# Performance work log

Measured on AMD Instinct MI355X. Metric: run time of the kernel, lower is better.

The kernel has to match this reference:

```python
import jax, jax.numpy as jnp
import numpy as np

# Standard minigrid color mapping (module references global COLOR_TO_IDX)
COLOR_TO_IDX = {'red': 0, 'green': 1, 'blue': 2, 'purple': 3, 'yellow': 4, 'grey': 5}
AGENT_FEATURE_SIZE = 13
NUM_AGENTS_PER_COLOR = {'grey': 4, 'yellow': 4}
COLOR_ORDER = sorted(NUM_AGENTS_PER_COLOR.keys())  # ['grey', 'yellow']
FEATURE_DIM = 256
B, N = 131072, 16
INPUT_DIM = (1 + sum(NUM_AGENTS_PER_COLOR.values())) * AGENT_FEATURE_SIZE  # 117


def setup_inputs() -> dict:
    key = jax.random.key(0)
    ks = jax.random.split(key, 14)
    inp = {
        'query_position': jax.random.normal(ks[0], (B, 2), jnp.float32),
        'query_direction': jax.random.normal(ks[1], (B, 4), jnp.float32),
        'query_abilities': jax.random.normal(ks[2], (B, 2), jnp.float32),
        'query_carried': jax.random.normal(ks[3], (B, 2), jnp.float32),
        'query_status': jax.random.normal(ks[4], (B, 3), jnp.float32),
        'all_agent_positions': jax.random.normal(ks[5], (B, N, 2), jnp.float32),
        'all_agent_directions': jax.random.normal(ks[6], (B, N, 4), jnp.float32),
        'all_agent_abilities': jax.random.normal(ks[7], (B, N, 2), jnp.float32),
        'all_agent_carried': jax.random.normal(ks[8], (B, N, 2), jnp.float32),
        'all_agent_status': jax.random.normal(ks[9], (B, N, 3), jnp.float32),
        'agent_color_indices': jax.random.randint(ks[10], (B, N), 0, 6, jnp.int32),
        # fc params; W stored (in, out) so y = x @ W + b (same math as torch Linear)
        'W': jax.random.normal(ks[11], (INPUT_DIM, FEATURE_DIM), jnp.float32) / np.sqrt(INPUT_DIM),
        'b': jax.random.normal(ks[12], (FEATURE_DIM,), jnp.float32) * 0.01,
    }
    return inp


def reference(query_position, query_direction, query_abilities, query_carried,
              query_status, all_agent_positions, all_agent_directions,
              all_agent_abilities, all_agent_carried, all_agent_status,
              agent_color_indices, W, b):
    batch = query_position.shape[0]
    # (B, N, 13) per-agent features, (B, 13) query features
    F = jnp.concatenate([all_agent_positions, all_agent_directions,
                         all_agent_abilities, all_agent_carried,
                         all_agent_status], axis=-1)
    query = jnp.concatenate([query_position, query_direction, query_abilities,
                             query_carried, query_status], axis=-1)
    feats = [query]
    rows = jnp.arange(batch)[:, None]  # (B, 1) for batched scatter
    for color in COLOR_ORDER:
        cidx = COLOR_TO_IDX[color]
        M = NUM_AGENTS_PER_COLOR[color]
        mask = agent_color_indices == cidx                 # (B, N)
        rank = jnp.cumsum(mask, axis=1) - 1                # slot of each matching agent
        valid = mask & (rank < M)
        slot = jnp.where(valid, rank, M)                   # dump overflow/non-match into slot M
        out = jnp.zeros((batch, M + 1, AGENT_FEATURE_SIZE), F.dtype)
        out = out.at[rows, slot].set(F)                    # unique (b, slot) per valid agent
        feats.append(out[:, :M].reshape(batch, M * AGENT_FEATURE_SIZE))
    x = jnp.concatenate(feats, axis=1)                     # (B, 117)
    return jax.nn.relu(x @ W + b)
```

## Files before the change

kernel.cpp:

```cpp
#include <hip/hip_runtime.h>


#define TM 128
#define XS_LD 136
#define THREADS 512
#define NCOL 256
#define KDIM 117

typedef short short8 __attribute__((ext_vector_type(8)));
typedef float f32x4 __attribute__((ext_vector_type(4)));

__device__ __forceinline__ short f2bf(float x) {
    unsigned u = __builtin_bit_cast(unsigned, x);
    unsigned r = (u + 0x7fffu + ((u >> 16) & 1u)) >> 16;
    return (short)r;
}

__global__ __launch_bounds__(THREADS, 2)
void mga_encoder_kernel(const float* __restrict__ qpos, const float* __restrict__ qdir,
                        const float* __restrict__ qabil, const float* __restrict__ qcarr,
                        const float* __restrict__ qstat,
                        const float* __restrict__ apos, const float* __restrict__ adir,
                        const float* __restrict__ aabil, const float* __restrict__ acarr,
                        const float* __restrict__ astat,
                        const int* __restrict__ cidx,
                        const float* __restrict__ W, const float* __restrict__ bvec,
                        float* __restrict__ out) {
    __shared__ __align__(16) short Xs[TM * XS_LD];

    const int tid  = threadIdx.x;
    const int wave = tid >> 6;
    const int lane = tid & 63;
    const int ln   = lane & 15;
    const int q    = lane >> 4;
    const int row0 = blockIdx.x * TM;

    const int r0w = (wave & 1) * 64;
    const int c0  = (wave >> 1) * 64;

    short8 bfr[4][4];
    #pragma unroll
    for (int kt = 0; kt < 4; kt++) {
        #pragma unroll
        for (int ct = 0; ct < 4; ct++) {
            short8 f;
            #pragma unroll
            for (int j = 0; j < 8; j++) {
                int k = kt * 32 + q * 8 + j;
                float wv = (k < KDIM) ? W[(size_t)k * NCOL + c0 + ct * 16 + ln] : 0.f;
                f[j] = f2bf(wv);
            }
            bfr[kt][ct] = f;
        }
    }
    float bv[4];
    #pragma unroll
    for (int ct = 0; ct < 4; ct++) bv[ct] = bvec[c0 + ct * 16 + ln];

    {
        unsigned* z = (unsigned*)Xs;
        #pragma unroll
        for (int i = 0; i < 17; i++) z[tid + THREADS * i] = 0u;
    }
    __syncthreads();

    {
        const int j  = tid & 15;
        const int rr = tid >> 4;
        const int grp = lane & 0x30;
        const unsigned long long rowmask = 0xFFFFull << grp;
        const unsigned long long below   = (1ull << lane) - 1ull;

        int cs[4];
        #pragma unroll
        for (int p = 0; p < 4; p++)
            cs[p] = cidx[((size_t)(row0 + p * 32 + rr)) * 16 + j];

        #pragma unroll
        for (int p = 0; p < 4; p++) {
            const int r = p * 32 + rr;
            const size_t b = (size_t)(row0 + r);
            const int c = cs[p];
            const bool isg = (c == 5);
            const bool isy = (c == 4);
            const unsigned long long bg = __ballot(isg);
            const unsigned long long by = __ballot(isy);
            if (isg | isy) {
                const unsigned long long bal = isg ? bg : by;
                const int rank = __popcll(bal & rowmask & below);
                if (rank < 4) {
                    const int dst = (isg ? 13 : 65) + rank * 13;
                    short* xrow = &Xs[r * XS_LD];
                    const size_t a = b * 16 + (size_t)j;
                    const float2 pp  = ((const float2*)apos)[a];
                    const float4 dd  = ((const float4*)adir)[a];
                    const float2 ab  = ((const float2*)aabil)[a];
                    const float2 ca  = ((const float2*)acarr)[a];
                    const float s0 = astat[a * 3 + 0];
                    const float s1 = astat[a * 3 + 1];
                    const float s2 = astat[a * 3 + 2];
                    xrow[dst + 0]  = f2bf(pp.x);
                    xrow[dst + 1]  = f2bf(pp.y);
                    xrow[dst + 2]  = f2bf(dd.x);
                    xrow[dst + 3]  = f2bf(dd.y);
                    xrow[dst + 4]  = f2bf(dd.z);
                    xrow[dst + 5]  = f2bf(dd.w);
                    xrow[dst + 6]  = f2bf(ab.x);
                    xrow[dst + 7]  = f2bf(ab.y);
                    xrow[dst + 8]  = f2bf(ca.x);
                    xrow[dst + 9]  = f2bf(ca.y);
                    xrow[dst + 10] = f2bf(s0);
                    xrow[dst + 11] = f2bf(s1);
                    xrow[dst + 12] = f2bf(s2);
                }
            }
        }
    }
    if (tid < TM) {
        const size_t b = (size_t)(row0 + tid);
        short* xrow = &Xs[tid * XS_LD];
        const float2 qp = ((const float2*)qpos)[b];
        const float4 qd = ((const float4*)qdir)[b];
        const float2 qa = ((const float2*)qabil)[b];
        const float2 qc = ((const float2*)qcarr)[b];
        const float s0 = qstat[b * 3 + 0];
        const float s1 = qstat[b * 3 + 1];
        const float s2 = qstat[b * 3 + 2];
        xrow[0]  = f2bf(qp.x);  xrow[1]  = f2bf(qp.y);
        xrow[2]  = f2bf(qd.x);  xrow[3]  = f2bf(qd.y);
        xrow[4]  = f2bf(qd.z);  xrow[5]  = f2bf(qd.w);
        xrow[6]  = f2bf(qa.x);  xrow[7]  = f2bf(qa.y);
        xrow[8]  = f2bf(qc.x);  xrow[9]  = f2bf(qc.y);
        xrow[10] = f2bf(s0);    xrow[11] = f2bf(s1);    xrow[12] = f2bf(s2);
    }
    __syncthreads();

    f32x4 acc[4][4];
    #pragma unroll
    for (int rt = 0; rt < 4; rt++)
        #pragma unroll
        for (int ct = 0; ct < 4; ct++) acc[rt][ct] = (f32x4){0.f, 0.f, 0.f, 0.f};

    #pragma unroll
    for (int kt = 0; kt < 4; kt++) {
        short8 av[4];
        #pragma unroll
        for (int rt = 0; rt < 4; rt++)
            av[rt] = *(const short8*)&Xs[(r0w + rt * 16 + ln) * XS_LD + kt * 32 + q * 8];
        #pragma unroll
        for (int rt = 0; rt < 4; rt++)
            #pragma unroll
            for (int ct = 0; ct < 4; ct++)
                acc[rt][ct] = __builtin_amdgcn_mfma_f32_16x16x32_bf16(
                    av[rt], bfr[kt][ct], acc[rt][ct], 0, 0, 0);
    }

    #pragma unroll
    for (int rt = 0; rt < 4; rt++) {
        #pragma unroll
        for (int ct = 0; ct < 4; ct++) {
            #pragma unroll
            for (int i = 0; i < 4; i++) {
                int row = row0 + r0w + rt * 16 + q * 4 + i;
                int col = c0 + ct * 16 + ln;
                float v = acc[rt][ct][i] + bv[ct];
                out[(size_t)row * NCOL + col] = fmaxf(v, 0.f);
            }
        }
    }
}

extern "C" void kernel_launch(void* const* d_in, const int* in_sizes, int n_in,
                              void* d_out, int out_size, void* d_ws, size_t ws_size,
                              hipStream_t stream) {
    const float* qpos  = (const float*)d_in[0];
    const float* qdir  = (const float*)d_in[1];
    const float* qabil = (const float*)d_in[2];
    const float* qcarr = (const float*)d_in[3];
    const float* qstat = (const float*)d_in[4];
    const float* apos  = (const float*)d_in[5];
    const float* adir  = (const float*)d_in[6];
    const float* aabil = (const float*)d_in[7];
    const float* acarr = (const float*)d_in[8];
    const float* astat = (const float*)d_in[9];
    const int*   cidx  = (const int*)d_in[10];
    const float* W     = (const float*)d_in[11];
    const float* bvec  = (const float*)d_in[12];
    float* out = (float*)d_out;

    const int B = in_sizes[0] / 2;
    const int nblocks = B / TM;

    mga_encoder_kernel<<<nblocks, THREADS, 0, stream>>>(
        qpos, qdir, qabil, qcarr, qstat, apos, adir, aabil, acarr, astat,
        cidx, W, bvec, out);
}
```

Measured before the change: 265.6 us.

## Persistent grid with pre-swizzled bf16 weights, slot-gather fill, vectorized nontemporal stores

A small pre-kernel converts W to bf16 in the MFMA fragment layout, using 14-wide padded agent slots, and stores it in the workspace. The main kernel now runs as a persistent grid of at most 512 blocks looping over row chunks. Per row chunk, each slot thread finds its k-th matching agent with ballot bit tricks and writes packed bf16 pairs, which removes the separate LDS zero pass. The GEMM swaps operands so each lane holds 4 consecutive columns, allowing float4 nontemporal output stores. Weights are reloaded per half-tile, 8 fragments instead of 16, to cut registers and allow 4 blocks per CU, at the cost of repeated fragment loads and an extra launch.

```diff
diff --git a/kernel.cpp b/kernel.cpp
--- a/kernel.cpp
+++ b/kernel.cpp
@@ -5,7 +5,7 @@
 #define XS_LD 136
 #define THREADS 512
 #define NCOL 256
-#define KDIM 117
+#define GRIDMAX 512
 
 typedef short short8 __attribute__((ext_vector_type(8)));
 typedef float f32x4 __attribute__((ext_vector_type(4)));
@@ -15,8 +15,29 @@
     unsigned r = (u + 0x7fffu + ((u >> 16) & 1u)) >> 16;
     return (short)r;
 }
-
-__global__ __launch_bounds__(THREADS, 2)
+__device__ __forceinline__ unsigned pk2(float a, float b) {
+    return (unsigned)(unsigned short)f2bf(a) | ((unsigned)(unsigned short)f2bf(b) << 16);
+}
+
+__global__ __launch_bounds__(256)
+void swz_w_kernel(const float* __restrict__ W, short* __restrict__ Wb) {
+    const int idx  = blockIdx.x * 256 + threadIdx.x;
+    const int j    = idx & 7;
+    const int lane = (idx >> 3) & 63;
+    const int ct   = (idx >> 9) & 3;
+    const int kt   = (idx >> 11) & 3;
+    const int cg   = (idx >> 13) & 3;
+    const int kk   = kt * 32 + (lane >> 4) * 8 + j;
+    const int u    = kk / 14;
+    const int f    = kk - u * 14;
+    const int col  = cg * 64 + ct * 16 + (lane & 15);
+    float v = 0.f;
+    if (u < 9 && f < 13) v = W[(u * 13 + f) * NCOL + col];
+    Wb[idx] = f2bf(v);
+}
+
+template<bool WS>
+__global__ __launch_bounds__(THREADS, 4)
 void mga_encoder_kernel(const float* __restrict__ qpos, const float* __restrict__ qdir,
                         const float* __restrict__ qabil, const float* __restrict__ qcarr,
                         const float* __restrict__ qstat,
@@ -25,7 +46,8 @@
                         const float* __restrict__ astat,
                         const int* __restrict__ cidx,
                         const float* __restrict__ W, const float* __restrict__ bvec,
-                        float* __restrict__ out) {
+                        const short* __restrict__ Wb,
+                        float* __restrict__ out, int nchunks) {
     __shared__ __align__(16) short Xs[TM * XS_LD];
 
     const int tid  = threadIdx.x;
@@ -33,140 +55,152 @@
     const int lane = tid & 63;
     const int ln   = lane & 15;
     const int q    = lane >> 4;
-    const int row0 = blockIdx.x * TM;
-
-    const int r0w = (wave & 1) * 64;
-    const int c0  = (wave >> 1) * 64;
-
-    short8 bfr[4][4];
+    const int r0w  = (wave & 1) * 64;
+    const int cg   = wave >> 1;
+    const int c0   = cg * 64;
+
     #pragma unroll
-    for (int kt = 0; kt < 4; kt++) {
-        #pragma unroll
-        for (int ct = 0; ct < 4; ct++) {
-            short8 f;
-            #pragma unroll
-            for (int j = 0; j < 8; j++) {
-                int k = kt * 32 + q * 8 + j;
-                float wv = (k < KDIM) ? W[(size_t)k * NCOL + c0 + ct * 16 + ln] : 0.f;
-                f[j] = f2bf(wv);
-            }
-            bfr[kt][ct] = f;
+    for (int i = tid; i < TM * 5; i += THREADS) {
+        const int row = i / 5, w = i - row * 5;
+        *(unsigned*)&Xs[row * XS_LD + 126 + w * 2] = 0u;
+    }
+
+    const int rr  = tid >> 4;
+    const int u   = tid & 15;
+    const int grp = tid & 48;
+
+    const short8* Wf = (const short8*)Wb;
+
+    #pragma unroll 1
+    for (int t = blockIdx.x; t < nchunks; t += gridDim.x) {
+        const int rowbase = t * TM;
+
+        if (tid < TM) {
+            const size_t b = (size_t)(rowbase + tid);
+            const float2 qp = ((const float2*)qpos)[b];
+            const float4 qd = ((const float4*)qdir)[b];
+            const float2 qa = ((const float2*)qabil)[b];
+            const float2 qc = ((const float2*)qcarr)[b];
+            const float s0 = qstat[b * 3 + 0];
+            const float s1 = qstat[b * 3 + 1];
+            const float s2 = qstat[b * 3 + 2];
+            unsigned* xd = (unsigned*)&Xs[tid * XS_LD];
+            xd[0] = pk2(qp.x, qp.y); xd[1] = pk2(qd.x, qd.y);
+            xd[2] = pk2(qd.z, qd.w); xd[3] = pk2(qa.x, qa.y);
+            xd[4] = pk2(qc.x, qc.y); xd[5] = pk2(s0, s1);
+            xd[6] = pk2(s2, 0.f);
         }
-    }
-    float bv[4];
-    #pragma unroll
-    for (int ct = 0; ct < 4; ct++) bv[ct] = bvec[c0 + ct * 16 + ln];
-
-    {
-        unsigned* z = (unsigned*)Xs;
-        #pragma unroll
-        for (int i = 0; i < 17; i++) z[tid + THREADS * i] = 0u;
-    }
-    __syncthreads();
-
-    {
-        const int j  = tid & 15;
-        const int rr = tid >> 4;
-        const int grp = lane & 0x30;
-        const unsigned long long rowmask = 0xFFFFull << grp;
-        const unsigned long long below   = (1ull << lane) - 1ull;
 
         int cs[4];
         #pragma unroll
         for (int p = 0; p < 4; p++)
-            cs[p] = cidx[((size_t)(row0 + p * 32 + rr)) * 16 + j];
+            cs[p] = cidx[((size_t)(rowbase + p * 32 + rr)) * 16 + u];
 
         #pragma unroll
         for (int p = 0; p < 4; p++) {
             const int r = p * 32 + rr;
-            const size_t b = (size_t)(row0 + r);
+            const size_t b = (size_t)(rowbase + r);
             const int c = cs[p];
-            const bool isg = (c == 5);
-            const bool isy = (c == 4);
-            const unsigned long long bg = __ballot(isg);
-            const unsigned long long by = __ballot(isy);
-            if (isg | isy) {
-                const unsigned long long bal = isg ? bg : by;
-                const int rank = __popcll(bal & rowmask & below);
-                if (rank < 4) {
-                    const int dst = (isg ? 13 : 65) + rank * 13;
-                    short* xrow = &Xs[r * XS_LD];
+            const unsigned long long bg = __ballot(c == 5);
+            const unsigned long long by = __ballot(c == 4);
+            if (u >= 1 && u <= 8) {
+                unsigned mm = (unsigned)(((u <= 4) ? bg : by) >> grp) & 0xFFFFu;
+                const int rank = (u - 1) & 3;
+                mm = (rank > 0) ? (mm & (mm - 1)) : mm;
+                mm = (rank > 1) ? (mm & (mm - 1)) : mm;
+                mm = (rank > 2) ? (mm & (mm - 1)) : mm;
+                const int j = mm ? (__ffs(mm) - 1) : -1;
+                float f0=0.f,f1=0.f,f2=0.f,f3=0.f,f4=0.f,f5=0.f,f6=0.f,
+                      f7=0.f,f8=0.f,f9=0.f,f10=0.f,f11=0.f,f12=0.f;
+                if (j >= 0) {
                     const size_t a = b * 16 + (size_t)j;
-                    const float2 pp  = ((const float2*)apos)[a];
-                    const float4 dd  = ((const float4*)adir)[a];
-                    const float2 ab  = ((const float2*)aabil)[a];
-                    const float2 ca  = ((const float2*)acarr)[a];
-                    const float s0 = astat[a * 3 + 0];
-                    const float s1 = astat[a * 3 + 1];
-                    const float s2 = astat[a * 3 + 2];
-                    xrow[dst + 0]  = f2bf(pp.x);
-                    xrow[dst + 1]  = f2bf(pp.y);
-                    xrow[dst + 2]  = f2bf(dd.x);
-                    xrow[dst + 3]  = f2bf(dd.y);
-                    xrow[dst + 4]  = f2bf(dd.z);
-                    xrow[dst + 5]  = f2bf(dd.w);
-                    xrow[dst + 6]  = f2bf(ab.x);
-                    xrow[dst + 7]  = f2bf(ab.y);
-                    xrow[dst + 8]  = f2bf(ca.x);
-                    xrow[dst + 9]  = f2bf(ca.y);
-                    xrow[dst + 10] = f2bf(s0);
-                    xrow[dst + 11] = f2bf(s1);
-                    xrow[dst + 12] = f2bf(s2);
+                    const float2 pp = ((const float2*)apos)[a];
+                    const float4 dd = ((const float4*)adir)[a];
+                    const float2 ab = ((const float2*)aabil)[a];
+                    const float2 ca = ((const float2*)acarr)[a];
+                    f0 = pp.x; f1 = pp.y;
+                    f2 = dd.x; f3 = dd.y; f4 = dd.z; f5 = dd.w;
+                    f6 = ab.x; f7 = ab.y; f8 = ca.x; f9 = ca.y;
+                    f10 = astat[a * 3 + 0]; f11 = astat[a * 3 + 1]; f12 = astat[a * 3 + 2];
                 }
+                unsigned* xd = (unsigned*)&Xs[r * XS_LD + 14 * u];
+                xd[0] = pk2(f0, f1);   xd[1] = pk2(f2, f3);
+                xd[2] = pk2(f4, f5);   xd[3] = pk2(f6, f7);
+                xd[4] = pk2(f8, f9);   xd[5] = pk2(f10, f11);
+                xd[6] = pk2(f12, 0.f);
             }
         }
-    }
-    if (tid < TM) {
-        const size_t b = (size_t)(row0 + tid);
-        short* xrow = &Xs[tid * XS_LD];
-        const float2 qp = ((const float2*)qpos)[b];
-        const float4 qd = ((const float4*)qdir)[b];
-        const float2 qa = ((const float2*)qabil)[b];
-        const float2 qc = ((const float2*)qcarr)[b];
-        const float s0 = qstat[b * 3 + 0];
-        const float s1 = qstat[b * 3 + 1];
-        const float s2 = qstat[b * 3 + 2];
-        xrow[0]  = f2bf(qp.x);  xrow[1]  = f2bf(qp.y);
-        xrow[2]  = f2bf(qd.x);  xrow[3]  = f2bf(qd.y);
-        xrow[4]  = f2bf(qd.z);  xrow[5]  = f2bf(qd.w);
-        xrow[6]  = f2bf(qa.x);  xrow[7]  = f2bf(qa.y);
-        xrow[8]  = f2bf(qc.x);  xrow[9]  = f2bf(qc.y);
-        xrow[10] = f2bf(s0);    xrow[11] = f2bf(s1);    xrow[12] = f2bf(s2);
-    }
-    __syncthreads();
-
-    f32x4 acc[4][4];
-    #pragma unroll
-    for (int rt = 0; rt < 4; rt++)
-        #pragma unroll
-        for (int ct = 0; ct < 4; ct++) acc[rt][ct] = (f32x4){0.f, 0.f, 0.f, 0.f};
-
-    #pragma unroll
-    for (int kt = 0; kt < 4; kt++) {
-        short8 av[4];
-        #pragma unroll
-        for (int rt = 0; rt < 4; rt++)
-            av[rt] = *(const short8*)&Xs[(r0w + rt * 16 + ln) * XS_LD + kt * 32 + q * 8];
-        #pragma unroll
-        for (int rt = 0; rt < 4; rt++)
-            #pragma unroll
-            for (int ct = 0; ct < 4; ct++)
-                acc[rt][ct] = __builtin_amdgcn_mfma_f32_16x16x32_bf16(
-                    av[rt], bfr[kt][ct], acc[rt][ct], 0, 0, 0);
-    }
-
-    #pragma unroll
-    for (int rt = 0; rt < 4; rt++) {
-        #pragma unroll
-        for (int ct = 0; ct < 4; ct++) {
-            #pragma unroll
-            for (int i = 0; i < 4; i++) {
-                int row = row0 + r0w + rt * 16 + q * 4 + i;
-                int col = c0 + ct * 16 + ln;
-                float v = acc[rt][ct][i] + bv[ct];
-                out[(size_t)row * NCOL + col] = fmaxf(v, 0.f);
+        __syncthreads();
+
+        #pragma unroll 1
+        for (int h = 0; h < 2; h++) {
+            short8 bfr[4][2];
+            if constexpr (WS) {
+                #pragma unroll
+                for (int kt = 0; kt < 4; kt++)
+                    #pragma unroll
+                    for (int cc = 0; cc < 2; cc++)
+                        bfr[kt][cc] = Wf[((cg * 4 + kt) * 4 + 2 * h + cc) * 64 + lane];
+            } else {
+                #pragma unroll
+                for (int kt = 0; kt < 4; kt++)
+                    #pragma unroll
+                    for (int cc = 0; cc < 2; cc++) {
+                        short8 fr;
+                        #pragma unroll
+                        for (int j = 0; j < 8; j++) {
+                            const int kk = kt * 32 + q * 8 + j;
+                            const int uu = kk / 14;
+                            const int ff = kk - uu * 14;
+                            float v = 0.f;
+                            if (uu < 9 && ff < 13)
+                                v = W[(uu * 13 + ff) * NCOL + c0 + (2 * h + cc) * 16 + ln];
+                            fr[j] = f2bf(v);
+                        }
+                        bfr[kt][cc] = fr;
+                    }
+            }
+            f32x4 bv[2];
+            #pragma unroll
+            for (int cc = 0; cc < 2; cc++)
+                bv[cc] = *(const f32x4*)&bvec[c0 + (2 * h + cc) * 16 + q * 4];
+
+            f32x4 acc[4][2];
+            #pragma unroll
+            for (int rt = 0; rt < 4; rt++)
+                #pragma unroll
+                for (int cc = 0; cc < 2; cc++) acc[rt][cc] = (f32x4){0.f, 0.f, 0.f, 0.f};
+
+            #pragma unroll
+            for (int kt = 0; kt < 4; kt++) {
+                short8 av[4];
+                #pragma unroll
+                for (int rt = 0; rt < 4; rt++)
+                    av[rt] = *(const short8*)&Xs[(r0w + rt * 16 + ln) * XS_LD + kt * 32 + q * 8];
+                #pragma unroll
+                for (int rt = 0; rt < 4; rt++)
+                    #pragma unroll
+                    for (int cc = 0; cc < 2; cc++)
+                        acc[rt][cc] = __builtin_amdgcn_mfma_f32_16x16x32_bf16(
+                            bfr[kt][cc], av[rt], acc[rt][cc], 0, 0, 0);
+            }
+
+            #pragma unroll
+            for (int rt = 0; rt < 4; rt++) {
+                const int row = rowbase + r0w + rt * 16 + ln;
+                #pragma unroll
+                for (int cc = 0; cc < 2; cc++) {
+                    const int col = c0 + (2 * h + cc) * 16 + q * 4;
+                    f32x4 v;
+                    v[0] = fmaxf(acc[rt][cc][0] + bv[cc][0], 0.f);
+                    v[1] = fmaxf(acc[rt][cc][1] + bv[cc][1], 0.f);
+                    v[2] = fmaxf(acc[rt][cc][2] + bv[cc][2], 0.f);
+                    v[3] = fmaxf(acc[rt][cc][3] + bv[cc][3], 0.f);
+                    __builtin_nontemporal_store(v, (f32x4*)&out[(size_t)row * NCOL + col]);
+                }
             }
         }
+        __syncthreads();
     }
 }
 
@@ -189,9 +223,18 @@
     float* out = (float*)d_out;
 
     const int B = in_sizes[0] / 2;
-    const int nblocks = B / TM;
-
-    mga_encoder_kernel<<<nblocks, THREADS, 0, stream>>>(
-        qpos, qdir, qabil, qcarr, qstat, apos, adir, aabil, acarr, astat,
-        cidx, W, bvec, out);
-}
+    const int nchunks = B / TM;
+    const int grid = nchunks < GRIDMAX ? nchunks : GRIDMAX;
+
+    const bool ws_ok = (d_ws != nullptr) && (ws_size >= 32768 * sizeof(short));
+    if (ws_ok) {
+        swz_w_kernel<<<128, 256, 0, stream>>>(W, (short*)d_ws);
+        mga_encoder_kernel<true><<<grid, THREADS, 0, stream>>>(
+            qpos, qdir, qabil, qcarr, qstat, apos, adir, aabil, acarr, astat,
+            cidx, W, bvec, (const short*)d_ws, out, nchunks);
+    } else {
+        mga_encoder_kernel<false><<<grid, THREADS, 0, stream>>>(
+            qpos, qdir, qabil, qcarr, qstat, apos, adir, aabil, acarr, astat,
+            cidx, W, bvec, nullptr, out, nchunks);
+    }
+}
```

Result: slower. 284.4 us (+7.1%).
